# Optimization experiments

Measured on AMD Instinct MI355X. Metric: run time of the kernel, lower is better.

The kernel has to match this reference:

```python
import jax, jax.numpy as jnp
import numpy as np

D_MODEL = 1024
NUM_HEADS = 16
D_HEAD = D_MODEL // NUM_HEADS
B, T = 2, 2048


def setup_inputs() -> dict:
    key = jax.random.key(0)
    k1, k2, k3 = jax.random.split(key, 3)
    std_qkv = np.sqrt(2.0 / (3 * D_MODEL + D_MODEL))
    std_out = np.sqrt(2.0 / (D_MODEL + D_MODEL))
    x = jax.random.normal(k1, (B, T, D_MODEL), dtype=jnp.float32)
    Wqkv = jax.random.normal(k2, (3 * D_MODEL, D_MODEL), dtype=jnp.float32) * std_qkv
    Wout = jax.random.normal(k3, (D_MODEL, D_MODEL), dtype=jnp.float32) * std_out
    return {"x": x, "Wqkv": Wqkv, "Wout": Wout}


def reference(x, Wqkv, Wout):
    Bz, Tz, _ = x.shape
    qkv = jnp.einsum('btd,ed->bte', x, Wqkv)  # [B,T,3*d_model]
    q, k, v = jnp.split(qkv, 3, axis=-1)
    # [B,T,H,Dh] -> [B,H,T,Dh]
    def to_heads(t):
        return t.reshape(Bz, Tz, NUM_HEADS, D_HEAD).transpose(0, 2, 1, 3)
    q, k, v = to_heads(q), to_heads(k), to_heads(v)
    scale = 1.0 / jnp.sqrt(jnp.asarray(D_HEAD, dtype=x.dtype))
    scores = jnp.einsum('bhqd,bhkd->bhqk', q, k) * scale
    causal = jnp.tril(jnp.ones((Tz, Tz), dtype=bool))
    scores = jnp.where(causal, scores, -jnp.inf)
    weights = jax.nn.softmax(scores, axis=-1)
    y = jnp.einsum('bhqk,bhkd->bhqd', weights, v)
    y = y.transpose(0, 2, 1, 3).reshape(Bz, Tz, D_MODEL)
    return jnp.einsum('btd,ed->bte', y, Wout)
```

## Files before the change

kernel.cpp:

```cpp
#include <hip/hip_runtime.h>
#include <hip/hip_bf16.h>

#define B_SZ    2
#define T_SEQ   2048
#define D_MODEL 1024
#define N_HEADS 16
#define D_HEAD  64
#define BT      (B_SZ * T_SEQ)

typedef unsigned short u16;
typedef __attribute__((ext_vector_type(8))) short  short8;
typedef __attribute__((ext_vector_type(4))) float  floatx4;
typedef __attribute__((ext_vector_type(4))) unsigned short ushortx4;

__device__ inline u16 f2b(float f) {
    __hip_bfloat16 h = __float2bfloat16(f);
    return *(u16*)&h;
}

__device__ inline void gld_lds16(const void* g, void* l) {
    __builtin_amdgcn_global_load_lds(
        (const __attribute__((address_space(1))) void*)g,
        (__attribute__((address_space(3))) void*)l, 16, 0, 0);
}

__global__ __launch_bounds__(256) void cvt3_kernel(
    const float* __restrict__ x, const float* __restrict__ wq,
    const float* __restrict__ wo,
    u16* __restrict__ xb, u16* __restrict__ wqb, u16* __restrict__ wob)
{
    const int n4x = (BT * D_MODEL) / 4;
    const int n4q = (3 * D_MODEL * D_MODEL) / 4;
    const int n4o = (D_MODEL * D_MODEL) / 4;
    int i = blockIdx.x * 256 + threadIdx.x;
    const float* src; u16* dst;
    if (i < n4x)            { src = x;  dst = xb;  }
    else if (i < n4x + n4q) { i -= n4x; src = wq; dst = wqb; }
    else                    { i -= n4x + n4q; if (i >= n4o) return; src = wo; dst = wob; }
    floatx4 v = ((const floatx4*)src)[i];
    ushortx4 r;
    r[0] = f2b(v[0]); r[1] = f2b(v[1]); r[2] = f2b(v[2]); r[3] = f2b(v[3]);
    ((ushortx4*)dst)[i] = r;
}

template <int EPI>
__global__ __launch_bounds__(256) void gemm_tile_kernel(
    const u16* __restrict__ A, const u16* __restrict__ B, int N, int K,
    float* __restrict__ C, u16* __restrict__ Qb, u16* __restrict__ Kb,
    u16* __restrict__ Vt)
{
    __shared__ __align__(16) u16 Ab[128][32];
    __shared__ __align__(16) u16 Bb[128][32];

    const int tid  = threadIdx.x;
    const int w    = tid >> 6;
    const int lane = tid & 63;
    const int col  = lane & 15;
    const int quad = lane >> 4;
    const int wm   = w & 1;
    const int wn   = w >> 1;

    const int tm = blockIdx.x & 31;
    const int tn = blockIdx.x >> 5;

    const int r0 = w * 32;
    const int lr = lane >> 2;
    const int ls = (lane & 3) << 3;
    const u16* gA0 = A + (size_t)(tm * 128 + r0 + lr) * K + ls;
    const u16* gA1 = gA0 + (size_t)16 * K;
    const u16* gB0 = B + (size_t)(tn * 128 + r0 + lr) * K + ls;
    const u16* gB1 = gB0 + (size_t)16 * K;
    u16* lA0 = &Ab[r0][0];
    u16* lA1 = &Ab[r0 + 16][0];
    u16* lB0 = &Bb[r0][0];
    u16* lB1 = &Bb[r0 + 16][0];

    floatx4 acc[4][4];
    #pragma unroll
    for (int i = 0; i < 4; ++i)
        #pragma unroll
        for (int j = 0; j < 4; ++j) acc[i][j] = (floatx4){0.f, 0.f, 0.f, 0.f};

    for (int k0 = 0; k0 < K; k0 += 32) {
        __syncthreads();
        gld_lds16(gA0 + k0, lA0);
        gld_lds16(gA1 + k0, lA1);
        gld_lds16(gB0 + k0, lB0);
        gld_lds16(gB1 + k0, lB1);
        __syncthreads();

        short8 af[4], bf[4];
        #pragma unroll
        for (int mt = 0; mt < 4; ++mt)
            af[mt] = *(const short8*)&Ab[wm * 64 + mt * 16 + col][quad * 8];
        #pragma unroll
        for (int nt = 0; nt < 4; ++nt)
            bf[nt] = *(const short8*)&Bb[wn * 64 + nt * 16 + col][quad * 8];
        #pragma unroll
        for (int mt = 0; mt < 4; ++mt)
            #pragma unroll
            for (int nt = 0; nt < 4; ++nt)
                acc[mt][nt] = __builtin_amdgcn_mfma_f32_16x16x32_bf16(
                    af[mt], bf[nt], acc[mt][nt], 0, 0, 0);
    }

    #pragma unroll
    for (int nt = 0; nt < 4; ++nt) {
        const int gcol = tn * 128 + wn * 64 + nt * 16 + col;
        #pragma unroll
        for (int mt = 0; mt < 4; ++mt) {
            #pragma unroll
            for (int rr = 0; rr < 4; ++rr) {
                const int m = tm * 128 + wm * 64 + mt * 16 + quad * 4 + rr;
                const float v = acc[mt][nt][rr];
                if (EPI == 1) {
                    C[(size_t)m * N + gcol] = v;
                } else {
                    const int sec = gcol >> 10;
                    const int h   = (gcol >> 6) & 15;
                    const int d   = gcol & 63;
                    const int bb  = m >> 11;
                    const int tl  = m & (T_SEQ - 1);
                    if (sec == 0)
                        Qb[((size_t)(bb * N_HEADS + h) * T_SEQ + tl) * D_HEAD + d] = f2b(v * 0.125f);
                    else if (sec == 1)
                        Kb[((size_t)(bb * N_HEADS + h) * T_SEQ + tl) * D_HEAD + d] = f2b(v);
                    else
                        Vt[((size_t)(bb * N_HEADS + h) * D_HEAD + d) * T_SEQ + tl] = f2b(v);
                }
            }
        }
    }
}

__global__ __launch_bounds__(256) void attn_mfma_kernel(
    const u16* __restrict__ Qb, const u16* __restrict__ Kb,
    const u16* __restrict__ Vt, u16* __restrict__ y)
{
    const int bid = blockIdx.x;
    const int qt  = 31 - (bid >> 5);
    const int h   = (bid >> 1) & 15;
    const int b   = bid & 1;
    const int bh  = b * N_HEADS + h;

    __shared__ __align__(16) u16 KV[2][2][64][64];
    __shared__ __align__(16) u16 Pl[4][16][72];

    const int tid  = threadIdx.x;
    const int w    = tid >> 6;
    const int lane = tid & 63;
    const int col  = lane & 15;
    const int quad = lane >> 4;

    const int srl  = lane >> 3;
    const int sseg = ((lane & 7) ^ srl) << 3;
    const int row0 = w * 16 + srl;
    const u16* kbase = Kb + (size_t)bh * T_SEQ * D_HEAD;
    const u16* vbase = Vt + (size_t)bh * D_HEAD * T_SEQ;
    const size_t offK0 = (size_t)row0 * D_HEAD + sseg;
    const size_t offK1 = offK0 + (size_t)8 * D_HEAD;
    const size_t offV0 = (size_t)row0 * T_SEQ + sseg;
    const size_t offV1 = offV0 + (size_t)8 * T_SEQ;

    short8 qf0, qf1;
    {
        const u16* qp = Qb + ((size_t)(bh * T_SEQ + qt * 64 + w * 16 + col)) * D_HEAD + quad * 8;
        qf0 = *(const short8*)qp;
        qf1 = *(const short8*)(qp + 32);
    }

    float m_s = -INFINITY;
    float l_s = 0.f;
    floatx4 O[4];
    #pragma unroll
    for (int dt = 0; dt < 4; ++dt) O[dt] = (floatx4){0.f, 0.f, 0.f, 0.f};

    const int c7 = col & 7;
    const int sA = (quad ^ c7) << 3;
    const int sB = ((quad ^ c7) ^ 4) << 3;

    gld_lds16(kbase + offK0, &KV[0][0][w * 16][0]);
    gld_lds16(kbase + offK1, &KV[0][0][w * 16 + 8][0]);
    gld_lds16(vbase + offV0, &KV[0][1][w * 16][0]);
    gld_lds16(vbase + offV1, &KV[0][1][w * 16 + 8][0]);

    for (int kt = 0; kt <= qt; ++kt) {
        __syncthreads();

        if (kt < qt) {
            const int nb = (kt + 1) & 1;
            const u16* kt_k = kbase + (size_t)(kt + 1) * 64 * D_HEAD;
            const u16* kt_v = vbase + (size_t)(kt + 1) * 64;
            gld_lds16(kt_k + offK0, &KV[nb][0][w * 16][0]);
            gld_lds16(kt_k + offK1, &KV[nb][0][w * 16 + 8][0]);
            gld_lds16(kt_v + offV0, &KV[nb][1][w * 16][0]);
            gld_lds16(kt_v + offV1, &KV[nb][1][w * 16 + 8][0]);
        }

        const u16 (*Ksb)[64] = KV[kt & 1][0];
        const u16 (*Vsb)[64] = KV[kt & 1][1];

        const bool diag  = (kt == qt);
        const int  ctmax = diag ? w : 3;

        floatx4 S[4];
        #pragma unroll
        for (int ct = 0; ct < 4; ++ct) {
            if (ct <= ctmax) {
                const u16* kp = &Ksb[ct * 16 + col][0];
                short8 k0 = *(const short8*)(kp + sA);
                short8 k1 = *(const short8*)(kp + sB);
                floatx4 acc = {0.f, 0.f, 0.f, 0.f};
                acc = __builtin_amdgcn_mfma_f32_16x16x32_bf16(k0, qf0, acc, 0, 0, 0);
                acc = __builtin_amdgcn_mfma_f32_16x16x32_bf16(k1, qf1, acc, 0, 0, 0);
                if (diag && ct == ctmax) {
                    #pragma unroll
                    for (int r = 0; r < 4; ++r)
                        if (quad * 4 + r > col) acc[r] = -1e30f;
                }
                S[ct] = acc;
            } else {
                S[ct] = (floatx4){-1e30f, -1e30f, -1e30f, -1e30f};
            }
        }

        floatx4 mv;
        #pragma unroll
        for (int r = 0; r < 4; ++r)
            mv[r] = fmaxf(fmaxf(S[0][r], S[1][r]), fmaxf(S[2][r], S[3][r]));
        float mloc = fmaxf(fmaxf(mv[0], mv[1]), fmaxf(mv[2], mv[3]));
        mloc = fmaxf(mloc, __shfl_xor(mloc, 16));
        mloc = fmaxf(mloc, __shfl_xor(mloc, 32));
        const float mnew  = fmaxf(m_s, mloc);
        const float alpha = __expf(m_s - mnew);
        m_s = mnew;

        float rs = 0.f;
        #pragma unroll
        for (int ct = 0; ct < 4; ++ct) {
            #pragma unroll
            for (int r = 0; r < 4; ++r) {
                float p = __expf(S[ct][r] - mnew);
                S[ct][r] = p;
                rs += p;
            }
        }
        rs += __shfl_xor(rs, 16);
        rs += __shfl_xor(rs, 32);
        l_s = l_s * alpha + rs;

        float a_row[4];
        #pragma unroll
        for (int r = 0; r < 4; ++r) a_row[r] = __shfl(alpha, quad * 4 + r);
        #pragma unroll
        for (int dt = 0; dt < 4; ++dt)
            #pragma unroll
            for (int r = 0; r < 4; ++r) O[dt][r] *= a_row[r];

        #pragma unroll
        for (int ct = 0; ct < 4; ++ct) {
            ushortx4 pk;
            pk[0] = f2b(S[ct][0]); pk[1] = f2b(S[ct][1]);
            pk[2] = f2b(S[ct][2]); pk[3] = f2b(S[ct][3]);
            *(ushortx4*)&Pl[w][col][ct * 16 + quad * 4] = pk;
        }

        const int kchunks = diag ? ((ctmax * 16 + 15) >> 5) : 1;
        #pragma unroll
        for (int c = 0; c < 2; ++c) {
            if (c <= kchunks) {
                short8 pa = *(const short8*)&Pl[w][col][c * 32 + quad * 8];
                #pragma unroll
                for (int dt = 0; dt < 4; ++dt) {
                    const u16* vp = &Vsb[dt * 16 + col][0];
                    short8 vb = *(const short8*)(vp + (c ? sB : sA));
                    O[dt] = __builtin_amdgcn_mfma_f32_16x16x32_bf16(pa, vb, O[dt], 0, 0, 0);
                }
            }
        }
    }

    float inv_row[4];
    #pragma unroll
    for (int r = 0; r < 4; ++r) inv_row[r] = 1.0f / __shfl(l_s, quad * 4 + r);
    #pragma unroll
    for (int dt = 0; dt < 4; ++dt) {
        #pragma unroll
        for (int r = 0; r < 4; ++r) {
            const size_t q_g = (size_t)(b * T_SEQ + qt * 64 + w * 16 + quad * 4 + r);
            y[q_g * D_MODEL + h * D_HEAD + dt * 16 + col] = f2b(O[dt][r] * inv_row[r]);
        }
    }
}

extern "C" void kernel_launch(void* const* d_in, const int* in_sizes, int n_in,
                              void* d_out, int out_size, void* d_ws, size_t ws_size,
                              hipStream_t stream) {
    const float* x    = (const float*)d_in[0];
    const float* Wqkv = (const float*)d_in[1];
    const float* Wout = (const float*)d_in[2];
    float* out = (float*)d_out;

    u16* xb    = (u16*)d_ws;
    u16* wqkvb = (u16*)((char*)d_ws + ( 8u << 20));
    u16* woutb = (u16*)((char*)d_ws + (14u << 20));
    u16* Qb    = (u16*)((char*)d_ws + (16u << 20));
    u16* Kb    = (u16*)((char*)d_ws + (24u << 20));
    u16* Vtb   = (u16*)((char*)d_ws + (32u << 20));
    u16* yb    = (u16*)((char*)d_ws + (40u << 20));

    cvt3_kernel<<<8192, 256, 0, stream>>>(x, Wqkv, Wout, xb, wqkvb, woutb);

    gemm_tile_kernel<0><<<32 * (3 * D_MODEL / 128), 256, 0, stream>>>(
        xb, wqkvb, 3 * D_MODEL, D_MODEL, nullptr, Qb, Kb, Vtb);

    attn_mfma_kernel<<<B_SZ * N_HEADS * (T_SEQ / 64), 256, 0, stream>>>(Qb, Kb, Vtb, yb);

    gemm_tile_kernel<1><<<32 * (D_MODEL / 128), 256, 0, stream>>>(
        yb, woutb, D_MODEL, D_MODEL, out, nullptr, nullptr, nullptr);
}
```

Measured before the change: 190.6 us.

## Split long causal attention rows across two blocks and retile output GEMM

```diff
diff --git a/kernel.cpp b/kernel.cpp
--- a/kernel.cpp
+++ b/kernel.cpp
@@ -43,12 +43,11 @@
     ((ushortx4*)dst)[i] = r;
 }
 
-template <int EPI>
-__global__ __launch_bounds__(256) void gemm_tile_kernel(
-    const u16* __restrict__ A, const u16* __restrict__ B, int N, int K,
-    float* __restrict__ C, u16* __restrict__ Qb, u16* __restrict__ Kb,
-    u16* __restrict__ Vt)
+__global__ __launch_bounds__(256) void gemm_qkv_kernel(
+    const u16* __restrict__ A, const u16* __restrict__ B,
+    u16* __restrict__ Qb, u16* __restrict__ Kb, u16* __restrict__ Vt)
 {
+    const int K = D_MODEL;
     __shared__ __align__(16) u16 Ab[128][32];
     __shared__ __align__(16) u16 Bb[128][32];
 
@@ -107,41 +106,111 @@
     #pragma unroll
     for (int nt = 0; nt < 4; ++nt) {
         const int gcol = tn * 128 + wn * 64 + nt * 16 + col;
+        const int sec = gcol >> 10;
+        const int h   = (gcol >> 6) & 15;
+        const int d   = gcol & 63;
         #pragma unroll
         for (int mt = 0; mt < 4; ++mt) {
             #pragma unroll
             for (int rr = 0; rr < 4; ++rr) {
-                const int m = tm * 128 + wm * 64 + mt * 16 + quad * 4 + rr;
+                const int m  = tm * 128 + wm * 64 + mt * 16 + quad * 4 + rr;
+                const int bb = m >> 11;
+                const int tl = m & (T_SEQ - 1);
                 const float v = acc[mt][nt][rr];
-                if (EPI == 1) {
-                    C[(size_t)m * N + gcol] = v;
-                } else {
-                    const int sec = gcol >> 10;
-                    const int h   = (gcol >> 6) & 15;
-                    const int d   = gcol & 63;
-                    const int bb  = m >> 11;
-                    const int tl  = m & (T_SEQ - 1);
-                    if (sec == 0)
-                        Qb[((size_t)(bb * N_HEADS + h) * T_SEQ + tl) * D_HEAD + d] = f2b(v * 0.125f);
-                    else if (sec == 1)
-                        Kb[((size_t)(bb * N_HEADS + h) * T_SEQ + tl) * D_HEAD + d] = f2b(v);
-                    else
-                        Vt[((size_t)(bb * N_HEADS + h) * D_HEAD + d) * T_SEQ + tl] = f2b(v);
-                }
-            }
-        }
+                if (sec == 0)
+                    Qb[((size_t)(bb * N_HEADS + h) * T_SEQ + tl) * D_HEAD + d] = f2b(v * 0.125f);
+                else if (sec == 1)
+                    Kb[((size_t)(bb * N_HEADS + h) * T_SEQ + tl) * D_HEAD + d] = f2b(v);
+                else
+                    Vt[((size_t)(bb * N_HEADS + h) * D_HEAD + d) * T_SEQ + tl] = f2b(v);
+            }
+        }
+    }
+}
+
+__global__ __launch_bounds__(256) void gemm_out_kernel(
+    const u16* __restrict__ A, const u16* __restrict__ B, float* __restrict__ C)
+{
+    const int K = D_MODEL, N = D_MODEL;
+    __shared__ __align__(16) u16 Ab[64][32];
+    __shared__ __align__(16) u16 Bb[128][32];
+
+    const int tid  = threadIdx.x;
+    const int w    = tid >> 6;
+    const int lane = tid & 63;
+    const int col  = lane & 15;
+    const int quad = lane >> 4;
+
+    const int tm = blockIdx.x & 63;
+    const int tn = blockIdx.x >> 6;
+
+    const int lr = lane >> 2;
+    const int ls = (lane & 3) << 3;
+    const u16* gA  = A + (size_t)(tm * 64 + w * 16 + lr) * K + ls;
+    const u16* gB0 = B + (size_t)(tn * 128 + w * 32 + lr) * K + ls;
+    const u16* gB1 = gB0 + (size_t)16 * K;
+    u16* lA  = &Ab[w * 16][0];
+    u16* lB0 = &Bb[w * 32][0];
+    u16* lB1 = &Bb[w * 32 + 16][0];
+
+    floatx4 acc[4][2];
+    #pragma unroll
+    for (int i = 0; i < 4; ++i) {
+        acc[i][0] = (floatx4){0.f, 0.f, 0.f, 0.f};
+        acc[i][1] = (floatx4){0.f, 0.f, 0.f, 0.f};
+    }
+
+    for (int k0 = 0; k0 < K; k0 += 32) {
+        __syncthreads();
+        gld_lds16(gA + k0, lA);
+        gld_lds16(gB0 + k0, lB0);
+        gld_lds16(gB1 + k0, lB1);
+        __syncthreads();
+
+        short8 af[4], bf[2];
+        #pragma unroll
+        for (int mt = 0; mt < 4; ++mt)
+            af[mt] = *(const short8*)&Ab[mt * 16 + col][quad * 8];
+        #pragma unroll
+        for (int nt = 0; nt < 2; ++nt)
+            bf[nt] = *(const short8*)&Bb[w * 32 + nt * 16 + col][quad * 8];
+        #pragma unroll
+        for (int mt = 0; mt < 4; ++mt)
+            #pragma unroll
+            for (int nt = 0; nt < 2; ++nt)
+                acc[mt][nt] = __builtin_amdgcn_mfma_f32_16x16x32_bf16(
+                    af[mt], bf[nt], acc[mt][nt], 0, 0, 0);
+    }
+
+    #pragma unroll
+    for (int nt = 0; nt < 2; ++nt) {
+        const int gcol = tn * 128 + w * 32 + nt * 16 + col;
+        #pragma unroll
+        for (int mt = 0; mt < 4; ++mt)
+            #pragma unroll
+            for (int rr = 0; rr < 4; ++rr) {
+                const int m = tm * 64 + mt * 16 + quad * 4 + rr;
+                C[(size_t)m * N + gcol] = acc[mt][nt][rr];
+            }
     }
 }
 
 __global__ __launch_bounds__(256) void attn_mfma_kernel(
     const u16* __restrict__ Qb, const u16* __restrict__ Kb,
-    const u16* __restrict__ Vt, u16* __restrict__ y)
+    const u16* __restrict__ Vt, u16* __restrict__ y,
+    float* __restrict__ Op, float* __restrict__ ml)
 {
     const int bid = blockIdx.x;
-    const int qt  = 31 - (bid >> 5);
-    const int h   = (bid >> 1) & 15;
-    const int b   = bid & 1;
-    const int bh  = b * N_HEADS + h;
+    const int bh  = bid & 31;
+    const int u   = bid >> 5;
+    int qt, s;
+    if (u < 32) { qt = 31 - (u >> 1); s = u & 1; }
+    else        { qt = 47 - u;        s = 0;     }
+    const int kt0 = s << 4;
+    const int kt1 = (s == 0) ? ((qt + 1 < 16) ? qt + 1 : 16) : (qt + 1);
+    const bool split = (qt >= 16);
+    const int b = bh >> 4;
+    const int h = bh & 15;
 
     __shared__ __align__(16) u16 KV[2][2][64][64];
     __shared__ __align__(16) u16 Pl[4][16][72];
@@ -179,15 +248,20 @@
     const int sA = (quad ^ c7) << 3;
     const int sB = ((quad ^ c7) ^ 4) << 3;
 
-    gld_lds16(kbase + offK0, &KV[0][0][w * 16][0]);
-    gld_lds16(kbase + offK1, &KV[0][0][w * 16 + 8][0]);
-    gld_lds16(vbase + offV0, &KV[0][1][w * 16][0]);
-    gld_lds16(vbase + offV1, &KV[0][1][w * 16 + 8][0]);
-
-    for (int kt = 0; kt <= qt; ++kt) {
+    {
+        const u16* kt_k = kbase + (size_t)kt0 * 64 * D_HEAD;
+        const u16* kt_v = vbase + (size_t)kt0 * 64;
+        const int nb = kt0 & 1;
+        gld_lds16(kt_k + offK0, &KV[nb][0][w * 16][0]);
+        gld_lds16(kt_k + offK1, &KV[nb][0][w * 16 + 8][0]);
+        gld_lds16(kt_v + offV0, &KV[nb][1][w * 16][0]);
+        gld_lds16(kt_v + offV1, &KV[nb][1][w * 16 + 8][0]);
+    }
+
+    for (int kt = kt0; kt < kt1; ++kt) {
         __syncthreads();
 
-        if (kt < qt) {
+        if (kt + 1 < kt1) {
             const int nb = (kt + 1) & 1;
             const u16* kt_k = kbase + (size_t)(kt + 1) * 64 * D_HEAD;
             const u16* kt_v = vbase + (size_t)(kt + 1) * 64;
@@ -237,14 +311,13 @@
 
         float rs = 0.f;
         #pragma unroll
-        for (int ct = 0; ct < 4; ++ct) {
+        for (int ct = 0; ct < 4; ++ct)
             #pragma unroll
             for (int r = 0; r < 4; ++r) {
                 float p = __expf(S[ct][r] - mnew);
                 S[ct][r] = p;
                 rs += p;
             }
-        }
         rs += __shfl_xor(rs, 16);
         rs += __shfl_xor(rs, 32);
         l_s = l_s * alpha + rs;
@@ -280,17 +353,62 @@
         }
     }
 
-    float inv_row[4];
-    #pragma unroll
-    for (int r = 0; r < 4; ++r) inv_row[r] = 1.0f / __shfl(l_s, quad * 4 + r);
-    #pragma unroll
-    for (int dt = 0; dt < 4; ++dt) {
-        #pragma unroll
-        for (int r = 0; r < 4; ++r) {
-            const size_t q_g = (size_t)(b * T_SEQ + qt * 64 + w * 16 + quad * 4 + r);
-            y[q_g * D_MODEL + h * D_HEAD + dt * 16 + col] = f2b(O[dt][r] * inv_row[r]);
-        }
-    }
+    if (!split) {
+        float inv_row[4];
+        #pragma unroll
+        for (int r = 0; r < 4; ++r) inv_row[r] = 1.0f / __shfl(l_s, quad * 4 + r);
+        #pragma unroll
+        for (int dt = 0; dt < 4; ++dt)
+            #pragma unroll
+            for (int r = 0; r < 4; ++r) {
+                const size_t q_g = (size_t)(b * T_SEQ + qt * 64 + w * 16 + quad * 4 + r);
+                y[q_g * D_MODEL + h * D_HEAD + dt * 16 + col] = f2b(O[dt][r] * inv_row[r]);
+            }
+    } else {
+        const int unit = (bh * 16 + (qt - 16)) * 2 + s;
+        if (quad == 0) {
+            float* mlp = ml + ((size_t)unit * 64 + w * 16 + col) * 2;
+            mlp[0] = m_s;
+            mlp[1] = l_s;
+        }
+        float* op = Op + (size_t)unit * 4096;
+        #pragma unroll
+        for (int dt = 0; dt < 4; ++dt)
+            #pragma unroll
+            for (int r = 0; r < 4; ++r)
+                op[(w * 16 + quad * 4 + r) * 64 + dt * 16 + col] = O[dt][r];
+    }
+}
+
+__global__ __launch_bounds__(256) void attn_merge_kernel(
+    const float* __restrict__ Op, const float* __restrict__ ml,
+    u16* __restrict__ y)
+{
+    const int idx  = blockIdx.x * 256 + threadIdx.x;
+    const int d4   = idx & 15;
+    const int q    = (idx >> 4) & 63;
+    const int qt16 = (idx >> 10) & 15;
+    const int bh   = idx >> 14;
+    const int unit0 = (bh * 16 + qt16) * 2;
+
+    const float* mlp1 = ml + ((size_t)unit0 * 64 + q) * 2;
+    const float* mlp2 = ml + ((size_t)(unit0 + 1) * 64 + q) * 2;
+    const float m1 = mlp1[0], l1 = mlp1[1];
+    const float m2 = mlp2[0], l2 = mlp2[1];
+    const float m  = fmaxf(m1, m2);
+    const float a1 = __expf(m1 - m), a2 = __expf(m2 - m);
+    const float inv = 1.0f / (l1 * a1 + l2 * a2);
+
+    const floatx4 o1 = *(const floatx4*)(Op + (size_t)unit0 * 4096 + q * 64 + d4 * 4);
+    const floatx4 o2 = *(const floatx4*)(Op + (size_t)(unit0 + 1) * 4096 + q * 64 + d4 * 4);
+
+    const int b = bh >> 4, h = bh & 15;
+    const size_t q_g = (size_t)(b * T_SEQ + (16 + qt16) * 64 + q);
+    ushortx4 r;
+    #pragma unroll
+    for (int j = 0; j < 4; ++j)
+        r[j] = f2b((o1[j] * a1 + o2[j] * a2) * inv);
+    *(ushortx4*)(y + q_g * D_MODEL + h * D_HEAD + d4 * 4) = r;
 }
 
 extern "C" void kernel_launch(void* const* d_in, const int* in_sizes, int n_in,
@@ -301,21 +419,24 @@
     const float* Wout = (const float*)d_in[2];
     float* out = (float*)d_out;
 
-    u16* xb    = (u16*)d_ws;
-    u16* wqkvb = (u16*)((char*)d_ws + ( 8u << 20));
-    u16* woutb = (u16*)((char*)d_ws + (14u << 20));
-    u16* Qb    = (u16*)((char*)d_ws + (16u << 20));
-    u16* Kb    = (u16*)((char*)d_ws + (24u << 20));
-    u16* Vtb   = (u16*)((char*)d_ws + (32u << 20));
-    u16* yb    = (u16*)((char*)d_ws + (40u << 20));
+    u16*  xb    = (u16*)d_ws;
+    u16*  wqkvb = (u16*)((char*)d_ws + ( 8u << 20));
+    u16*  woutb = (u16*)((char*)d_ws + (14u << 20));
+    u16*  Qb    = (u16*)((char*)d_ws + (16u << 20));
+    u16*  Kb    = (u16*)((char*)d_ws + (24u << 20));
+    u16*  Vtb   = (u16*)((char*)d_ws + (32u << 20));
+    u16*  yb    = (u16*)((char*)d_ws + (40u << 20));
+    float* Op   = (float*)((char*)d_ws + (48u << 20));
+    float* ml   = (float*)((char*)d_ws + (64u << 20));
 
     cvt3_kernel<<<8192, 256, 0, stream>>>(x, Wqkv, Wout, xb, wqkvb, woutb);
 
-    gemm_tile_kernel<0><<<32 * (3 * D_MODEL / 128), 256, 0, stream>>>(
-        xb, wqkvb, 3 * D_MODEL, D_MODEL, nullptr, Qb, Kb, Vtb);
-
-    attn_mfma_kernel<<<B_SZ * N_HEADS * (T_SEQ / 64), 256, 0, stream>>>(Qb, Kb, Vtb, yb);
-
-    gemm_tile_kernel<1><<<32 * (D_MODEL / 128), 256, 0, stream>>>(
-        yb, woutb, D_MODEL, D_MODEL, out, nullptr, nullptr, nullptr);
-}
+    gemm_qkv_kernel<<<32 * (3 * D_MODEL / 128), 256, 0, stream>>>(
+        xb, wqkvb, Qb, Kb, Vtb);
+
+    attn_mfma_kernel<<<32 * 48, 256, 0, stream>>>(Qb, Kb, Vtb, yb, Op, ml);
+
+    attn_merge_kernel<<<2048, 256, 0, stream>>>(Op, ml, yb);
+
+    gemm_out_kernel<<<512, 256, 0, stream>>>(yb, woutb, out);
+}
```

New measurement: 209.6 us. 1.1x slower.
